# Kernel tuning notes

Measured on AMD Instinct MI355X. Metric: run time of the kernel, lower is better.

The kernel has to match this reference:

```python
import jax, jax.numpy as jnp
import numpy as np
import math

# Single graph (batch vector identically 0): per-graph topk and global_max_pool
# reduce to static lax.top_k and jnp.max. Pooled edge_index from SAGPooling is
# discarded because KnnEdges rebuilds the graph every layer (no_op=False).
N = 20000      # nodes
HID = 128      # in_channels == hidden_channels
L = 3          # num_layers
RATIO = 0.5    # pool_ratio
K0, KINC = 6, 2  # KnnEdges start_k / k_increment
OUT = 5


def setup_inputs() -> dict:
    key = jax.random.key(0)
    ks = jax.random.split(key, 10)
    s = 0.05  # keep tanh scores unsaturated
    x = jax.random.normal(ks[0], (N, HID), jnp.float32)
    pos = jax.random.uniform(ks[1], (N, 2), jnp.float32) * 100.0
    src = jax.random.randint(ks[2], (N * K0,), 0, N)
    dst = jnp.repeat(jnp.arange(N), K0)
    edge_index = jnp.stack([src, dst]).astype(jnp.int32)  # [2, E], row0=src(j), row1=dst(i)
    return dict(
        x=x, pos=pos, edge_index=edge_index,
        Wrel=jax.random.normal(ks[3], (L, HID, HID), jnp.float32) * s,
        brel=jnp.zeros((L, HID), jnp.float32),
        Wroot=jax.random.normal(ks[4], (L, HID, HID), jnp.float32) * s,
        Wprel=jax.random.normal(ks[5], (L, HID), jnp.float32) * s,
        bprel=jnp.zeros((L,), jnp.float32),
        Wproot=jax.random.normal(ks[6], (L, HID), jnp.float32) * s,
        W1=jax.random.normal(ks[7], (HID * L, HID), jnp.float32) * s,
        b1=jnp.zeros((HID,), jnp.float32),
        W2=jax.random.normal(ks[8], (HID, OUT), jnp.float32) * s,
        b2=jnp.zeros((OUT,), jnp.float32),
    )


def _mean_agg(x, src, dst, n):
    # mean over incoming messages x_j for each target i (PyG aggr='mean'; 0 if isolated)
    ssum = jax.ops.segment_sum(x[src], dst, num_segments=n)
    deg = jax.ops.segment_sum(jnp.ones(src.shape, x.dtype), dst, num_segments=n)
    return ssum / jnp.maximum(deg, 1.0)[:, None]


def reference(x, pos, edge_index, Wrel, brel, Wroot, Wprel, bprel, Wproot, W1, b1, W2, b2):
    src, dst = edge_index[0], edge_index[1]
    n = x.shape[0]
    xs = []
    for i in range(L):
        # GraphConv(aggr='mean'): out_i = W_rel @ mean_j x_j + W_root @ x_i + b
        agg = _mean_agg(x, src, dst, n)
        x = jax.nn.relu(agg @ Wrel[i] + x @ Wroot[i] + brel[i])
        # SAGPooling: score GNN = GraphConv(hid->1, aggr='add'); tanh nonlinearity
        sagg = jax.ops.segment_sum(x[src], dst, num_segments=n)
        score = jnp.tanh(sagg @ Wprel[i] + x @ Wproot[i] + bprel[i])  # [n]
        k_keep = math.ceil(RATIO * n)
        vals, perm = jax.lax.top_k(score, k_keep)
        x = x[perm] * vals[:, None]
        xs.append(jnp.max(x, axis=0))  # global_max_pool (single graph)
        # KnnEdges: pos = pos[perm]; rebuild KNN graph with k = start_k + i*k_increment
        pos = pos[perm]
        n = k_keep
        k = K0 + KINC * i
        d2 = jnp.sum((pos[:, None, :] - pos[None, :, :]) ** 2, axis=-1)  # [n, n]
        d2 = jnp.where(jnp.eye(n, dtype=bool), jnp.inf, d2)  # loop=False
        _, nbr = jax.lax.top_k(-d2, k)  # [n, k] nearest neighbors
        src = nbr.reshape(-1)                 # neighbor j (source)
        dst = jnp.repeat(jnp.arange(n), k)    # query i (target)
    h = jnp.concatenate(xs)  # JumpingKnowledge mode='cat' -> [HID*L]
    h = jax.nn.relu(h @ W1 + b1)  # dropout p=0.5 in eval mode: identity
    return (h @ W2 + b2)[None, :]  # [1, OUT]
```

## Files before the change

kernel.cpp:

```cpp
#include <hip/hip_runtime.h>
#include <hip/hip_bf16.h>
#include <math.h>

#define HID 128
#define PR 20
#define CRPB 32
#define CAND_CAP 8192
#define MAXEQ 8192
#define MAXCELLS 4096

__device__ inline int wave_iscan(int v, int lane) {
#pragma unroll
  for (int off = 1; off < 64; off <<= 1) {
    int o = __shfl_up(v, off, 64);
    if (lane >= off) v += o;
  }
  return v;
}

template <int K>
__global__ __launch_bounds__(256) void k_conv_fused(
    const float* __restrict__ x, const int* __restrict__ src, int n, float invk,
    const float* __restrict__ Wrel, const float* __restrict__ Wroot,
    const float* __restrict__ brel,
    const float* __restrict__ wprel, const float* __restrict__ wproot,
    float* __restrict__ out, float* __restrict__ uo, float* __restrict__ vo) {
  __shared__ float4 sagg4[CRPB][HID / 4];
  __shared__ float4 sx4[CRPB][HID / 4];
  __shared__ int ssrc[CRPB * K];
  int t = threadIdx.x;
  int i0 = blockIdx.x * CRPB;
  const int nK = n * K;
  for (int s = t; s < CRPB * K; s += 256) {
    int gi = i0 * K + s;
    int v = (gi < nK) ? src[gi] : 0;
    ssrc[s] = ((unsigned)v < (unsigned)n) ? v : 0;
  }
  __syncthreads();
  {
    int fq = t & 31, h = t >> 5;
    const float4* x4 = (const float4*)x;
    for (int r = h; r < CRPB; r += 8) {
      int row = i0 + r;
      float4 s = make_float4(0.f, 0.f, 0.f, 0.f);
      float4 xv = make_float4(0.f, 0.f, 0.f, 0.f);
      if (row < n) {
#pragma unroll
        for (int j = 0; j < K; ++j) {
          float4 xx = x4[(size_t)ssrc[r * K + j] * 32 + fq];
          s.x += xx.x; s.y += xx.y; s.z += xx.z; s.w += xx.w;
        }
        xv = x4[(size_t)row * 32 + fq];
      }
      s.x *= invk; s.y *= invk; s.z *= invk; s.w *= invk;
      sagg4[r][fq] = s;
      sx4[r][fq] = xv;
    }
  }
  __syncthreads();
  int q = t & 31, rg = t >> 5;
  const float4* Wrel4  = (const float4*)Wrel;
  const float4* Wroot4 = (const float4*)Wroot;
  float4 bq = ((const float4*)brel)[q];
  float4 acc[4];
#pragma unroll
  for (int rr = 0; rr < 4; ++rr) acc[rr] = bq;
  int rbase = rg * 4;
#pragma unroll 2
  for (int cq = 0; cq < HID / 4; ++cq) {
    float4 w1[4], w2[4];
#pragma unroll
    for (int uu = 0; uu < 4; ++uu) {
      w1[uu] = Wrel4[(cq * 4 + uu) * 32 + q];
      w2[uu] = Wroot4[(cq * 4 + uu) * 32 + q];
    }
#pragma unroll
    for (int rr = 0; rr < 4; ++rr) {
      float4 a  = sagg4[rbase + rr][cq];
      float4 xx = sx4[rbase + rr][cq];
      acc[rr].x += a.x*w1[0].x + a.y*w1[1].x + a.z*w1[2].x + a.w*w1[3].x
                 + xx.x*w2[0].x + xx.y*w2[1].x + xx.z*w2[2].x + xx.w*w2[3].x;
      acc[rr].y += a.x*w1[0].y + a.y*w1[1].y + a.z*w1[2].y + a.w*w1[3].y
                 + xx.x*w2[0].y + xx.y*w2[1].y + xx.z*w2[2].y + xx.w*w2[3].y;
      acc[rr].z += a.x*w1[0].z + a.y*w1[1].z + a.z*w1[2].z + a.w*w1[3].z
                 + xx.x*w2[0].z + xx.y*w2[1].z + xx.z*w2[2].z + xx.w*w2[3].z;
      acc[rr].w += a.x*w1[0].w + a.y*w1[1].w + a.z*w1[2].w + a.w*w1[3].w
                 + xx.x*w2[0].w + xx.y*w2[1].w + xx.z*w2[2].w + xx.w*w2[3].w;
    }
  }
  float4 wplq = ((const float4*)wprel)[q];
  float4 wprq = ((const float4*)wproot)[q];
#pragma unroll
  for (int rr = 0; rr < 4; ++rr) {
    int row = i0 + rbase + rr;
    float4 v = acc[rr];
    v.x = v.x > 0.f ? v.x : 0.f;
    v.y = v.y > 0.f ? v.y : 0.f;
    v.z = v.z > 0.f ? v.z : 0.f;
    v.w = v.w > 0.f ? v.w : 0.f;
    float pu = 0.f, pv = 0.f;
    if (row < n) {
      ((float4*)out)[(size_t)row * 32 + q] = v;
      pu = v.x * wplq.x + v.y * wplq.y + v.z * wplq.z + v.w * wplq.w;
      pv = v.x * wprq.x + v.y * wprq.y + v.z * wprq.z + v.w * wprq.w;
    }
#pragma unroll
    for (int o = 16; o; o >>= 1) {
      pu += __shfl_down(pu, o, 32);
      pv += __shfl_down(pv, o, 32);
    }
    if (q == 0 && row < n) { uo[row] = pu; vo[row] = pv; }
  }
}

template <int K>
__global__ __launch_bounds__(256) void k_score_lite(
    const float* __restrict__ u, const float* __restrict__ v,
    const int* __restrict__ src, const float* __restrict__ bprel,
    int n, float* __restrict__ score, unsigned* __restrict__ key,
    unsigned* __restrict__ ghist) {
  __shared__ unsigned lh[1024];
  int t = threadIdx.x;
#pragma unroll
  for (int uu = 0; uu < 4; ++uu) lh[t + uu * 256] = 0u;
  __syncthreads();
  int i = blockIdx.x * 256 + t;
  if (i < n) {
    float s = v[i] + bprel[0];
#pragma unroll
    for (int j = 0; j < K; ++j) s += u[src[i * K + j]];
    float sc = tanhf(s);
    score[i] = sc;
    unsigned bb = __float_as_uint(sc);
    unsigned k2 = (bb & 0x80000000u) ? ~bb : (bb | 0x80000000u);
    key[i] = k2;
    atomicAdd(&lh[k2 >> 22], 1u);
  }
  __syncthreads();
#pragma unroll
  for (int uu = 0; uu < 4; ++uu) {
    unsigned vv = lh[t + uu * 256];
    if (vv) atomicAdd(&ghist[t + uu * 256], vv);
  }
}

__global__ __launch_bounds__(256) void k_collect(
    const unsigned* __restrict__ key, int n, int kk,
    const unsigned* __restrict__ ghist,
    unsigned* __restrict__ BA, unsigned* __restrict__ candbuf, int* __restrict__ candCnt) {
  __shared__ int wt[4];
  __shared__ unsigned shB, shAbove;
  int t = threadIdx.x;
  int lane = t & 63, wid = t >> 6;
  unsigned h[4]; int s = 0;
#pragma unroll
  for (int uu = 0; uu < 4; ++uu) { h[uu] = ghist[t * 4 + uu]; s += (int)h[uu]; }
  int is = wave_iscan(s, lane);
  if (lane == 63) wt[wid] = is;
  __syncthreads();
  int b = 0, tot = 0;
#pragma unroll
  for (int w2 = 0; w2 < 4; ++w2) { int ss = wt[w2]; if (w2 < wid) b += ss; tot += ss; }
  int c = b + is - s;
#pragma unroll
  for (int uu = 0; uu < 4; ++uu) {
    c += (int)h[uu];
    unsigned above_strict = (unsigned)(tot - c);
    unsigned above_incl = above_strict + h[uu];
    if (above_incl >= (unsigned)kk && above_strict < (unsigned)kk) {
      shB = (unsigned)(t * 4 + uu);
      shAbove = above_strict;
    }
  }
  __syncthreads();
  unsigned B = shB;
  if (blockIdx.x == 0 && t == 0) { BA[0] = B; BA[1] = shAbove; }
  int i = blockIdx.x * 256 + t;
  unsigned long long lmask = (1ull << lane) - 1ull;
  unsigned kv = (i < n) ? key[i] : 0u;
  bool m = (i < n) && ((kv >> 22) == B);
  unsigned long long mm = __ballot(m);
  if (mm) {
    int leader = (int)(__ffsll((long long)mm) - 1);
    int base = 0;
    if (lane == leader) base = atomicAdd(candCnt, (int)__popcll(mm));
    base = __shfl(base, leader, 64);
    if (m) {
      int p = base + (int)__popcll(mm & lmask);
      if (p < CAND_CAP) candbuf[p] = kv;
    }
  }
}

__global__ __launch_bounds__(1024) void k_refine(const unsigned* __restrict__ candbuf,
                                                 const int* __restrict__ candCnt,
                                                 const unsigned* __restrict__ BA, int kk,
                                                 unsigned* __restrict__ outTG) {
  __shared__ unsigned cand[CAND_CAP];
  __shared__ unsigned hist256[256];
  __shared__ unsigned sh_remain, sh_prefix;
  __shared__ int wtB[4];
  int t = threadIdx.x;
  int lane = t & 63, wid = t >> 6;
  unsigned above = BA[1];
  int remain = kk - (int)above;
  int cnt = *candCnt; if (cnt > CAND_CAP) cnt = CAND_CAP;
  for (int i = t; i < cnt; i += 1024) cand[i] = candbuf[i];
  if (t == 0) { sh_prefix = 0u; sh_remain = (unsigned)remain; }
  __syncthreads();
  for (int pass = 0; pass < 4; ++pass) {
    int shift = 24 - pass * 8;
    unsigned prefix = sh_prefix;
    unsigned rem = sh_remain;
    if (t < 256) hist256[t] = 0u;
    __syncthreads();
    unsigned himask = (pass == 0) ? 0u : (0xFFFFFFFFu << (shift + 8));
    for (int i = t; i < cnt; i += 1024) {
      unsigned kky = cand[i];
      if ((kky & himask) == prefix) atomicAdd(&hist256[(kky >> shift) & 255u], 1u);
    }
    __syncthreads();
    int hv = (t < 256) ? (int)hist256[t] : 0;
    int iv = wave_iscan(hv, lane);
    if (t < 256 && lane == 63) wtB[wid] = iv;
    __syncthreads();
    if (t < 256) {
      int b = 0, tot = 0;
#pragma unroll
      for (int w2 = 0; w2 < 4; ++w2) { int s = wtB[w2]; if (w2 < wid) b += s; tot += s; }
      unsigned val = (unsigned)(iv + b);
      unsigned sstrict = (unsigned)tot - val;
      if (sstrict < rem && sstrict + (unsigned)hv >= rem) {
        sh_prefix = prefix | ((unsigned)t << shift);
        sh_remain = rem - sstrict;
      }
    }
    __syncthreads();
  }
  if (t == 0) {
    outTG[0] = sh_prefix;
    outTG[1] = above + (unsigned)remain - sh_remain;
  }
}

__global__ void k_sel(const unsigned* __restrict__ key, int n,
                      const unsigned* __restrict__ TG,
                      int* __restrict__ perm, int* __restrict__ cntGt,
                      int* __restrict__ eqbuf, int* __restrict__ cntEq) {
  int i = blockIdx.x * blockDim.x + threadIdx.x;
  int lane = threadIdx.x & 63;
  unsigned long long lmask = (1ull << lane) - 1ull;
  unsigned T = TG[0];
  unsigned kv = (i < n) ? key[i] : 0u;
  bool g = (i < n) && (kv > T);
  bool e = (i < n) && (kv == T);
  unsigned long long mg = __ballot(g);
  unsigned long long me = __ballot(e);
  if (mg) {
    int leader = (int)(__ffsll((long long)mg) - 1);
    int base = 0;
    if (lane == leader) base = atomicAdd(cntGt, (int)__popcll(mg));
    base = __shfl(base, leader, 64);
    if (g) perm[base + (int)__popcll(mg & lmask)] = i;
  }
  if (me) {
    int leader = (int)(__ffsll((long long)me) - 1);
    int base = 0;
    if (lane == leader) base = atomicAdd(cntEq, (int)__popcll(me));
    base = __shfl(base, leader, 64);
    if (e) {
      int p = base + (int)__popcll(me & lmask);
      if (p < MAXEQ) eqbuf[p] = i;
    }
  }
}

__global__ void k_sel_eq_fin(const unsigned* __restrict__ TG, const int* __restrict__ eqbuf,
                             const int* __restrict__ cntEq, int* __restrict__ perm, int kk) {
  int lane = threadIdx.x;
  int G = (int)TG[1];
  int need = kk - G;
  int cnt = *cntEq; if (cnt > MAXEQ) cnt = MAXEQ;
  int prev = -1;
  for (int t = 0; t < need; ++t) {
    int mymin = 0x7fffffff;
    for (int u = lane; u < cnt; u += 64) {
      int v = eqbuf[u];
      if (v > prev && v < mymin) mymin = v;
    }
    for (int o = 1; o < 64; o <<= 1) mymin = min(mymin, __shfl_xor(mymin, o, 64));
    if (lane == 0) perm[G + t] = mymin;
    prev = mymin;
  }
}

template <int R>
__global__ __launch_bounds__(256) void k_pool_pmax(
    const float* __restrict__ x, const float* __restrict__ score,
    const int* __restrict__ perm, const float* __restrict__ pos_in,
    float* __restrict__ xout, float* __restrict__ pos_out, int store,
    float* __restrict__ pmax, int* __restrict__ counts, int Gg, float inv_w) {
  __shared__ float sm[2][HID];
  int f = threadIdx.x & 127;
  int half = threadIdx.x >> 7;
  int j0 = blockIdx.x * R;
  float mx = -1e30f;
  for (int r = half; r < R; r += 2) {
    int j = j0 + r;
    int node = perm[j];
    float v = score[node];
    float val = x[(size_t)node * HID + f] * v;
    if (store) {
      xout[(size_t)j * HID + f] = val;
      if (f == 0) {
        float px = pos_in[node * 2], py = pos_in[node * 2 + 1];
        pos_out[j * 2] = px; pos_out[j * 2 + 1] = py;
        int cx = min(Gg - 1, max(0, (int)(px * inv_w)));
        int cy = min(Gg - 1, max(0, (int)(py * inv_w)));
        atomicAdd(&counts[cy * Gg + cx], 1);
      }
    }
    mx = fmaxf(mx, val);
  }
  sm[half][f] = mx;
  __syncthreads();
  if (half == 0) pmax[blockIdx.x * HID + f] = fmaxf(sm[0][f], sm[1][f]);
}

__global__ __launch_bounds__(1024) void k_grid_scan(const int* __restrict__ counts,
                                                    int* __restrict__ starts,
                                                    int* __restrict__ cursor, int cells) {
  __shared__ int wtA[16];
  int t = threadIdx.x;
  int lane = t & 63, wid = t >> 6;
  int c0[4]; int base4 = t * 4; int s = 0;
#pragma unroll
  for (int u = 0; u < 4; ++u) {
    int idx = base4 + u;
    c0[u] = (idx < cells) ? counts[idx] : 0;
    s += c0[u];
  }
  int is = wave_iscan(s, lane);
  if (lane == 63) wtA[wid] = is;
  __syncthreads();
  int b = 0;
#pragma unroll
  for (int w2 = 0; w2 < 16; ++w2) { if (w2 < wid) b += wtA[w2]; }
  int excl = b + is - s;
#pragma unroll
  for (int u = 0; u < 4; ++u) {
    int idx = base4 + u;
    if (idx < cells) { starts[idx] = excl; cursor[idx] = excl; excl += c0[u]; }
  }
}

__global__ void k_grid_scatter(const float2* __restrict__ pos, int m, int Gg, float inv_w,
                               int* __restrict__ cursor, float2* __restrict__ spos,
                               int* __restrict__ sidx) {
  int i = blockIdx.x * blockDim.x + threadIdx.x;
  if (i >= m) return;
  float2 p = pos[i];
  int cx = min(Gg - 1, max(0, (int)(p.x * inv_w)));
  int cy = min(Gg - 1, max(0, (int)(p.y * inv_w)));
  int pp = atomicAdd(&cursor[cy * Gg + cx], 1);
  spos[pp] = p;
  sidx[pp] = i;
}

template <int K>
__global__ __launch_bounds__(256) void k_knn_wave(const float2* __restrict__ spos,
                           const int* __restrict__ sidx,
                           const int* __restrict__ starts, const int* __restrict__ counts,
                           int m, int G, float w, float inv_w, int* __restrict__ src_out) {
  int lane = threadIdx.x & 63;
  int j = blockIdx.x * (blockDim.x >> 6) + (threadIdx.x >> 6);
  if (j >= m) return;
  float2 qp = spos[j];
  int q = sidx[j];
  int cx = min(G - 1, max(0, (int)(qp.x * inv_w)));
  int cy = min(G - 1, max(0, (int)(qp.y * inv_w)));

  float bd[K]; int bi[K];
#pragma unroll
  for (int t = 0; t < K; ++t) { bd[t] = 1e30f; bi[t] = 0; }

  auto scan_span = [&](int s, int e) {
    for (int p = s + lane; p < e; p += 64) {
      if (p == j) continue;
      float2 pp = spos[p];
      float dx = qp.x - pp.x, dy = qp.y - pp.y;
      float d = dx * dx + dy * dy;
      if (d < bd[K - 1]) {
        float dd = d; int ii = sidx[p];
#pragma unroll
        for (int t = 0; t < K; ++t) {
          bool sw = dd < bd[t];
          float od = bd[t]; int oi = bi[t];
          if (sw) { bd[t] = dd; bi[t] = ii; dd = od; ii = oi; }
        }
      }
    }
  };

  {
    int xl = max(0, cx - 1), xh = min(G - 1, cx + 1);
    int y0 = max(0, cy - 1), y1 = min(G - 1, cy + 1);
    int ss[3], ee[3]; int nr = 0;
    for (int y = y0; y <= y1; ++y) {
      int b = y * G;
      ss[nr] = starts[b + xl];
      ee[nr] = starts[b + xh] + counts[b + xh];
      ++nr;
    }
    for (int t = 0; t < nr; ++t) scan_span(ss[t], ee[t]);
  }

  int r = 1;
  unsigned long long mg[K];
  while (true) {
    unsigned long long tmp[K];
#pragma unroll
    for (int t = 0; t < K; ++t)
      tmp[t] = ((unsigned long long)__float_as_uint(bd[t]) << 32) | (unsigned)bi[t];
#pragma unroll
    for (int t = 0; t < K; ++t) {
      unsigned long long mn = tmp[0];
#pragma unroll
      for (int o = 1; o < 64; o <<= 1) {
        unsigned long long ot = __shfl_xor(mn, o, 64);
        if (ot < mn) mn = ot;
      }
      mg[t] = mn;
      if (tmp[0] == mn) {
#pragma unroll
        for (int s2 = 0; s2 < K - 1; ++s2) tmp[s2] = tmp[s2 + 1];
        tmp[K - 1] = ~0ull;
      }
    }
    float kth = __uint_as_float((unsigned)(mg[K - 1] >> 32));
    float bnd = 1e30f;
    if (cx - r > 0)     bnd = fminf(bnd, qp.x - (float)(cx - r) * w);
    if (cx + r < G - 1) bnd = fminf(bnd, (float)(cx + r + 1) * w - qp.x);
    if (cy - r > 0)     bnd = fminf(bnd, qp.y - (float)(cy - r) * w);
    if (cy + r < G - 1) bnd = fminf(bnd, (float)(cy + r + 1) * w - qp.y);
    if (bnd > 1e29f) break;
    float bb = fmaxf(bnd, 0.f) * 0.999f;
    if (kth < bb * bb) break;
    ++r;
    int xl = max(0, cx - r), xh = min(G - 1, cx + r);
    int yt = cy - r, yb = cy + r;
    if (yt >= 0)     { int b = yt * G; scan_span(starts[b + xl], starts[b + xh] + counts[b + xh]); }
    if (yb <= G - 1) { int b = yb * G; scan_span(starts[b + xl], starts[b + xh] + counts[b + xh]); }
    int ylo = max(0, cy - r + 1), yhi = min(G - 1, cy + r - 1);
    for (int y = ylo; y <= yhi; ++y) {
      int b = y * G;
      if (cx - r >= 0)     { int c = b + cx - r; scan_span(starts[c], starts[c] + counts[c]); }
      if (cx + r <= G - 1) { int c = b + cx + r; scan_span(starts[c], starts[c] + counts[c]); }
    }
  }
  if (lane == 0) {
#pragma unroll
    for (int t = 0; t < K; ++t) src_out[q * K + t] = (int)(unsigned)(mg[t] & 0xffffffffu);
  }
}

__global__ __launch_bounds__(256) void k_colmax2(const float* __restrict__ pmax,
                                                 int P0, int P1, int P2,
                                                 float* __restrict__ pmax2) {
  __shared__ float sm[2][HID];
  int l = blockIdx.x >> 3, c = blockIdx.x & 7;
  int lo3[3] = {0, P0, P0 + P1};
  int len3[3] = {P0, P1, P2};
  int lo = lo3[l], len = len3[l];
  int f = threadIdx.x & 127, half = threadIdx.x >> 7;
  float mx = -1e30f;
  for (int p = c + 8 * half; p < len; p += 16)
    mx = fmaxf(mx, pmax[(size_t)(lo + p) * HID + f]);
  sm[half][f] = mx;
  __syncthreads();
  if (half == 0) pmax2[(size_t)blockIdx.x * HID + f] = fmaxf(sm[0][f], sm[1][f]);
}

__global__ __launch_bounds__(1024) void k_final(const float* __restrict__ pmax2,
                        const float* __restrict__ W1, const float* __restrict__ b1,
                        const float* __restrict__ W2, const float* __restrict__ b2,
                        float* __restrict__ out) {
  __shared__ float sxs[3 * HID];
  __shared__ float red[8][HID];
  __shared__ float h1[HID];
  int f = threadIdx.x & 127, ch = threadIdx.x >> 7;
  if (ch < 3) {
    float mx = pmax2[(size_t)(ch * 8) * HID + f];
#pragma unroll
    for (int u = 1; u < 8; ++u) mx = fmaxf(mx, pmax2[(size_t)(ch * 8 + u) * HID + f]);
    sxs[ch * HID + f] = mx;
  }
  __syncthreads();
  float acc = 0.f;
  for (int c = ch * 48; c < (ch + 1) * 48; ++c) acc += sxs[c] * W1[c * HID + f];
  red[ch][f] = acc;
  __syncthreads();
  if (ch == 0) {
    float a = b1[f];
#pragma unroll
    for (int u = 0; u < 8; ++u) a += red[u][f];
    h1[f] = a > 0.f ? a : 0.f;
  }
  __syncthreads();
  if (threadIdx.x < 5) {
    float a = b2[threadIdx.x];
    for (int c = 0; c < HID; ++c) a += h1[c] * W2[c * 5 + threadIdx.x];
    out[threadIdx.x] = a;
  }
}

extern "C" void kernel_launch(void* const* d_in, const int* in_sizes, int n_in,
                              void* d_out, int out_size, void* d_ws, size_t ws_size,
                              hipStream_t stream) {
  const float* x_in   = (const float*)d_in[0];
  const float* pos_in = (const float*)d_in[1];
  const int*   ei     = (const int*)d_in[2];
  const float* Wrel   = (const float*)d_in[3];
  const float* brel   = (const float*)d_in[4];
  const float* Wroot  = (const float*)d_in[5];
  const float* Wprel  = (const float*)d_in[6];
  const float* bprel  = (const float*)d_in[7];
  const float* Wproot = (const float*)d_in[8];
  const float* W1     = (const float*)d_in[9];
  const float* b1     = (const float*)d_in[10];
  const float* W2     = (const float*)d_in[11];
  const float* b2     = (const float*)d_in[12];
  float* out = (float*)d_out;

  const int N0 = in_sizes[0] / HID;
  const int P0 = (N0 / 2) / PR, P1 = (N0 / 4) / PR, P2 = (N0 / 8) / PR;

  char* w = (char*)d_ws;
  float*    xB     = (float*)w;    w += (size_t)N0 * HID * 4;
  float*    xA     = (float*)w;    w += (size_t)(N0 / 2) * HID * 4;
  float*    score  = (float*)w;    w += (size_t)N0 * 4;
  unsigned* key    = (unsigned*)w; w += (size_t)N0 * 4;
  float*    ubuf   = (float*)w;    w += (size_t)N0 * 4;
  float*    vbuf   = (float*)w;    w += (size_t)N0 * 4;
  float*    posA   = (float*)w;    w += (size_t)(N0 / 2) * 2 * 4;
  float*    posB   = (float*)w;    w += (size_t)(N0 / 2) * 2 * 4;
  int*      srcbuf = (int*)w;      w += (size_t)(N0 / 2) * 8 * 4;
  int*      permb  = (int*)w;      w += (size_t)(N0 / 2) * 4;
  float*    pmax   = (float*)w;    w += (size_t)(P0 + P1 + P2) * HID * 4;
  float*    pmax2  = (float*)w;    w += (size_t)24 * HID * 4;
  unsigned* ghistB = (unsigned*)w; w += 3 * 1024 * 4;
  int*      cnt    = (int*)w;      w += 16 * 4;
  int*      countsB= (int*)w;      w += 2 * MAXCELLS * 4;
  const size_t ZERO_BYTES = 3 * 1024 * 4 + 16 * 4 + 2 * MAXCELLS * 4;
  unsigned* TG     = (unsigned*)w; w += 16;
  unsigned* BA     = (unsigned*)w; w += 16;
  unsigned* candbuf= (unsigned*)w; w += CAND_CAP * 4;
  int*      eqbuf  = (int*)w;      w += MAXEQ * 4;
  int*      starts = (int*)w;      w += MAXCELLS * 4;
  int*      cursor = (int*)w;      w += MAXCELLS * 4;
  float2*   spos   = (float2*)w;   w += (size_t)(N0 / 2) * 8;
  int*      sidx   = (int*)w;      w += (size_t)(N0 / 2) * 4;
  (void)ws_size; (void)n_in; (void)out_size;

  hipMemsetAsync(ghistB, 0, ZERO_BYTES, stream);

  int n = N0;
  const float* xcur   = x_in;
  const float* poscur = pos_in;
  const int*   srccur = ei;
  int kcur = 6;
  int Poff = 0;

  for (int l = 0; l < 3; ++l) {
    const int kk = n / 2;
    int Gg = (int)ceilf(sqrtf((float)kk / 2.5f));
    if (Gg > 64) Gg = 64;
    if (Gg < 1) Gg = 1;
    int cells = Gg * Gg;
    float cw = 100.f / (float)Gg;
    float inv_w = (float)Gg / 100.f;
    int cblocks = (n + CRPB - 1) / CRPB;
    unsigned* ghist = ghistB + l * 1024;
    int* counts = countsB + (l < 2 ? l : 0) * MAXCELLS;

    if (kcur == 6) {
      k_conv_fused<6><<<cblocks, 256, 0, stream>>>(xcur, srccur, n, 1.f / 6.f,
          Wrel + l * HID * HID, Wroot + l * HID * HID, brel + l * HID,
          Wprel + l * HID, Wproot + l * HID, xB, ubuf, vbuf);
      k_score_lite<6><<<(n + 255) / 256, 256, 0, stream>>>(ubuf, vbuf, srccur, bprel + l,
                                                           n, score, key, ghist);
    } else {
      k_conv_fused<8><<<cblocks, 256, 0, stream>>>(xcur, srccur, n, 1.f / 8.f,
          Wrel + l * HID * HID, Wroot + l * HID * HID, brel + l * HID,
          Wprel + l * HID, Wproot + l * HID, xB, ubuf, vbuf);
      k_score_lite<8><<<(n + 255) / 256, 256, 0, stream>>>(ubuf, vbuf, srccur, bprel + l,
                                                           n, score, key, ghist);
    }
    k_collect<<<(n + 255) / 256, 256, 0, stream>>>(key, n, kk, ghist, BA, candbuf, cnt + 3 * l + 2);
    k_refine<<<1, 1024, 0, stream>>>(candbuf, cnt + 3 * l + 2, BA, kk, TG);
    k_sel<<<(n + 255) / 256, 256, 0, stream>>>(key, n, TG, permb, cnt + 3 * l, eqbuf, cnt + 3 * l + 1);
    k_sel_eq_fin<<<1, 64, 0, stream>>>(TG, eqbuf, cnt + 3 * l + 1, permb, kk);

    float* pos_out = (l == 0) ? posA : posB;
    int store = (l < 2) ? 1 : 0;
    k_pool_pmax<PR><<<kk / PR, 256, 0, stream>>>(xB, score, permb, poscur, xA, pos_out,
                                                 store, pmax + (size_t)Poff * HID,
                                                 counts, Gg, inv_w);
    Poff += kk / PR;
    n = kk;
    if (l < 2) {
      k_grid_scan<<<1, 1024, 0, stream>>>(counts, starts, cursor, cells);
      k_grid_scatter<<<(n + 255) / 256, 256, 0, stream>>>((const float2*)pos_out, n, Gg, inv_w,
                                                          cursor, spos, sidx);
      if (l == 0) { k_knn_wave<6><<<(n + 3) / 4, 256, 0, stream>>>(spos, sidx, starts, counts,
                                                                   n, Gg, cw, inv_w, srcbuf); kcur = 6; }
      else        { k_knn_wave<8><<<(n + 3) / 4, 256, 0, stream>>>(spos, sidx, starts, counts,
                                                                   n, Gg, cw, inv_w, srcbuf); kcur = 8; }
    }
    xcur = xA; poscur = pos_out; srccur = srcbuf;
  }
  k_colmax2<<<24, 256, 0, stream>>>(pmax, P0, P1, P2, pmax2);
  k_final<<<1, 1024, 0, stream>>>(pmax2, W1, b1, W2, b2, out);
}
```

Measured before the change: 253.0 us.

## Break top-k ties with 64-bit key-index radix select, drop equal-key pass

Candidates now carry a 64-bit composite of the 32-bit score key and the inverted node index. The radix refine runs seven passes over this composite key to find an exact 64-bit threshold, so k_sel picks exactly k nodes with one ballot compaction. This removes the serial single-wave k_sel_eq_fin kernel, the equal-key buffer and one launch per layer. In exchange the refine kernel does more histogram passes over 64-bit candidates held in 64KB of dynamic shared memory.

```diff
diff --git a/kernel.cpp b/kernel.cpp
--- a/kernel.cpp
+++ b/kernel.cpp
@@ -6,7 +6,6 @@
 #define PR 20
 #define CRPB 32
 #define CAND_CAP 8192
-#define MAXEQ 8192
 #define MAXCELLS 4096
 
 __device__ inline int wave_iscan(int v, int lane) {
@@ -147,7 +146,8 @@
 __global__ __launch_bounds__(256) void k_collect(
     const unsigned* __restrict__ key, int n, int kk,
     const unsigned* __restrict__ ghist,
-    unsigned* __restrict__ BA, unsigned* __restrict__ candbuf, int* __restrict__ candCnt) {
+    unsigned* __restrict__ BA, unsigned long long* __restrict__ candbuf,
+    int* __restrict__ candCnt) {
   __shared__ int wt[4];
   __shared__ unsigned shB, shAbove;
   int t = threadIdx.x;
@@ -187,37 +187,44 @@
     base = __shfl(base, leader, 64);
     if (m) {
       int p = base + (int)__popcll(mm & lmask);
-      if (p < CAND_CAP) candbuf[p] = kv;
-    }
-  }
-}
-
-__global__ __launch_bounds__(1024) void k_refine(const unsigned* __restrict__ candbuf,
-                                                 const int* __restrict__ candCnt,
-                                                 const unsigned* __restrict__ BA, int kk,
-                                                 unsigned* __restrict__ outTG) {
-  __shared__ unsigned cand[CAND_CAP];
+      if (p < CAND_CAP) candbuf[p] = ((unsigned long long)kv << 32) | (unsigned)(~i);
+    }
+  }
+}
+
+__global__ __launch_bounds__(1024) void k_refine(
+    const unsigned long long* __restrict__ candbuf, const int* __restrict__ candCnt,
+    const unsigned* __restrict__ BA, int kk, unsigned long long* __restrict__ T64) {
+  extern __shared__ unsigned long long cands[];
   __shared__ unsigned hist256[256];
-  __shared__ unsigned sh_remain, sh_prefix;
+  __shared__ unsigned long long sh_prefix;
+  __shared__ unsigned sh_remain;
   __shared__ int wtB[4];
   int t = threadIdx.x;
   int lane = t & 63, wid = t >> 6;
-  unsigned above = BA[1];
-  int remain = kk - (int)above;
+  unsigned B = BA[0], above = BA[1];
   int cnt = *candCnt; if (cnt > CAND_CAP) cnt = CAND_CAP;
-  for (int i = t; i < cnt; i += 1024) cand[i] = candbuf[i];
-  if (t == 0) { sh_prefix = 0u; sh_remain = (unsigned)remain; }
-  __syncthreads();
-  for (int pass = 0; pass < 4; ++pass) {
-    int shift = 24 - pass * 8;
-    unsigned prefix = sh_prefix;
+  for (int i = t; i < cnt; i += 1024) cands[i] = candbuf[i];
+  if (t == 0) {
+    sh_prefix = ((unsigned long long)B) << 54;
+    sh_remain = (unsigned)(kk - (int)above);
+  }
+  __syncthreads();
+  const int shifts[7] = {46, 38, 30, 22, 14, 6, 0};
+  for (int p = 0; p < 7; ++p) {
+    int shift = shifts[p];
+    int bits = (p == 6) ? 6 : 8;
+    unsigned mask = (1u << bits) - 1u;
+    unsigned long long himask = (p == 0) ? (~0ull << 54)
+                                         : (~0ull << (shifts[p - 1]));
+    unsigned long long prefix = sh_prefix;
     unsigned rem = sh_remain;
     if (t < 256) hist256[t] = 0u;
     __syncthreads();
-    unsigned himask = (pass == 0) ? 0u : (0xFFFFFFFFu << (shift + 8));
     for (int i = t; i < cnt; i += 1024) {
-      unsigned kky = cand[i];
-      if ((kky & himask) == prefix) atomicAdd(&hist256[(kky >> shift) & 255u], 1u);
+      unsigned long long cc = cands[i];
+      if ((cc & himask) == prefix)
+        atomicAdd(&hist256[(unsigned)((cc >> shift) & mask)], 1u);
     }
     __syncthreads();
     int hv = (t < 256) ? (int)hist256[t] : 0;
@@ -230,67 +237,35 @@
       for (int w2 = 0; w2 < 4; ++w2) { int s = wtB[w2]; if (w2 < wid) b += s; tot += s; }
       unsigned val = (unsigned)(iv + b);
       unsigned sstrict = (unsigned)tot - val;
-      if (sstrict < rem && sstrict + (unsigned)hv >= rem) {
-        sh_prefix = prefix | ((unsigned)t << shift);
+      if ((unsigned)t <= mask && sstrict < rem && sstrict + (unsigned)hv >= rem) {
+        sh_prefix = prefix | ((unsigned long long)t << shift);
         sh_remain = rem - sstrict;
       }
     }
     __syncthreads();
   }
-  if (t == 0) {
-    outTG[0] = sh_prefix;
-    outTG[1] = above + (unsigned)remain - sh_remain;
-  }
+  if (t == 0) T64[0] = sh_prefix;
 }
 
 __global__ void k_sel(const unsigned* __restrict__ key, int n,
-                      const unsigned* __restrict__ TG,
-                      int* __restrict__ perm, int* __restrict__ cntGt,
-                      int* __restrict__ eqbuf, int* __restrict__ cntEq) {
+                      const unsigned long long* __restrict__ T64,
+                      int* __restrict__ perm, int* __restrict__ cntSel) {
   int i = blockIdx.x * blockDim.x + threadIdx.x;
   int lane = threadIdx.x & 63;
   unsigned long long lmask = (1ull << lane) - 1ull;
-  unsigned T = TG[0];
-  unsigned kv = (i < n) ? key[i] : 0u;
-  bool g = (i < n) && (kv > T);
-  bool e = (i < n) && (kv == T);
+  unsigned long long T = T64[0];
+  bool g = false;
+  if (i < n) {
+    unsigned long long k64 = ((unsigned long long)key[i] << 32) | (unsigned)(~i);
+    g = (k64 >= T);
+  }
   unsigned long long mg = __ballot(g);
-  unsigned long long me = __ballot(e);
   if (mg) {
     int leader = (int)(__ffsll((long long)mg) - 1);
     int base = 0;
-    if (lane == leader) base = atomicAdd(cntGt, (int)__popcll(mg));
+    if (lane == leader) base = atomicAdd(cntSel, (int)__popcll(mg));
     base = __shfl(base, leader, 64);
     if (g) perm[base + (int)__popcll(mg & lmask)] = i;
-  }
-  if (me) {
-    int leader = (int)(__ffsll((long long)me) - 1);
-    int base = 0;
-    if (lane == leader) base = atomicAdd(cntEq, (int)__popcll(me));
-    base = __shfl(base, leader, 64);
-    if (e) {
-      int p = base + (int)__popcll(me & lmask);
-      if (p < MAXEQ) eqbuf[p] = i;
-    }
-  }
-}
-
-__global__ void k_sel_eq_fin(const unsigned* __restrict__ TG, const int* __restrict__ eqbuf,
-                             const int* __restrict__ cntEq, int* __restrict__ perm, int kk) {
-  int lane = threadIdx.x;
-  int G = (int)TG[1];
-  int need = kk - G;
-  int cnt = *cntEq; if (cnt > MAXEQ) cnt = MAXEQ;
-  int prev = -1;
-  for (int t = 0; t < need; ++t) {
-    int mymin = 0x7fffffff;
-    for (int u = lane; u < cnt; u += 64) {
-      int v = eqbuf[u];
-      if (v > prev && v < mymin) mymin = v;
-    }
-    for (int o = 1; o < 64; o <<= 1) mymin = min(mymin, __shfl_xor(mymin, o, 64));
-    if (lane == 0) perm[G + t] = mymin;
-    prev = mymin;
   }
 }
 
@@ -552,10 +527,9 @@
   int*      cnt    = (int*)w;      w += 16 * 4;
   int*      countsB= (int*)w;      w += 2 * MAXCELLS * 4;
   const size_t ZERO_BYTES = 3 * 1024 * 4 + 16 * 4 + 2 * MAXCELLS * 4;
-  unsigned* TG     = (unsigned*)w; w += 16;
+  unsigned long long* T64 = (unsigned long long*)w; w += 16;
   unsigned* BA     = (unsigned*)w; w += 16;
-  unsigned* candbuf= (unsigned*)w; w += CAND_CAP * 4;
-  int*      eqbuf  = (int*)w;      w += MAXEQ * 4;
+  unsigned long long* candbuf = (unsigned long long*)w; w += CAND_CAP * 8;
   int*      starts = (int*)w;      w += MAXCELLS * 4;
   int*      cursor = (int*)w;      w += MAXCELLS * 4;
   float2*   spos   = (float2*)w;   w += (size_t)(N0 / 2) * 8;
@@ -596,10 +570,9 @@
       k_score_lite<8><<<(n + 255) / 256, 256, 0, stream>>>(ubuf, vbuf, srccur, bprel + l,
                                                            n, score, key, ghist);
     }
-    k_collect<<<(n + 255) / 256, 256, 0, stream>>>(key, n, kk, ghist, BA, candbuf, cnt + 3 * l + 2);
-    k_refine<<<1, 1024, 0, stream>>>(candbuf, cnt + 3 * l + 2, BA, kk, TG);
-    k_sel<<<(n + 255) / 256, 256, 0, stream>>>(key, n, TG, permb, cnt + 3 * l, eqbuf, cnt + 3 * l + 1);
-    k_sel_eq_fin<<<1, 64, 0, stream>>>(TG, eqbuf, cnt + 3 * l + 1, permb, kk);
+    k_collect<<<(n + 255) / 256, 256, 0, stream>>>(key, n, kk, ghist, BA, candbuf, cnt + 2 * l);
+    k_refine<<<1, 1024, CAND_CAP * 8, stream>>>(candbuf, cnt + 2 * l, BA, kk, T64);
+    k_sel<<<(n + 255) / 256, 256, 0, stream>>>(key, n, T64, permb, cnt + 2 * l + 1);
 
     float* pos_out = (l == 0) ? posA : posB;
     int store = (l < 2) ? 1 : 0;
```

Result: faster. 247.1 us (-2.3%).
